# Kernel tuning notes

Measured on AMD Instinct MI355X. Metric: run time of the kernel, lower is better.

Reference implementation:

```python
import jax, jax.numpy as jnp
from jax import lax
import numpy as np

D_MODEL = 1024
D_STATE = 16    # N
D_CONV = 4     # K
EXPAND = 2
D_INNER = EXPAND * D_MODEL          # E = 2048
DT_RANK = -(-D_MODEL // 16)         # ceil(D/16) = 64
BATCH, SEQLEN = 2, 1024


def setup_inputs() -> dict:
    key = jax.random.key(0)
    ks = jax.random.split(key, 12)
    s_in = 1.0 / np.sqrt(D_MODEL)
    s_e = 1.0 / np.sqrt(D_INNER)
    s_r = 1.0 / np.sqrt(DT_RANK)
    x = jax.random.normal(ks[0], (BATCH, SEQLEN, D_MODEL), jnp.float32)
    ln_g = jnp.ones((D_MODEL,), jnp.float32)
    ln_b = jnp.zeros((D_MODEL,), jnp.float32)
    W_in = jax.random.normal(ks[1], (D_MODEL, 2 * D_INNER), jnp.float32) * s_in
    conv_w = jax.random.normal(ks[2], (D_INNER, D_CONV), jnp.float32) * (1.0 / np.sqrt(D_CONV))
    conv_b = jnp.zeros((D_INNER,), jnp.float32)
    W_xp = jax.random.normal(ks[3], (D_INNER, DT_RANK + 2 * D_STATE), jnp.float32) * s_e
    W_dt = jax.random.normal(ks[4], (DT_RANK, D_INNER), jnp.float32) * s_r
    # dt bias init so softplus(b_dt) ~ U[1e-3, 1e-1] (official mamba init)
    dt = jnp.exp(jax.random.uniform(ks[5], (D_INNER,)) * (np.log(0.1) - np.log(1e-3)) + np.log(1e-3))
    b_dt = dt + jnp.log(-jnp.expm1(-dt))  # inverse softplus
    A_log = jnp.log(jnp.broadcast_to(jnp.arange(1, D_STATE + 1, dtype=jnp.float32), (D_INNER, D_STATE)))
    D_param = jnp.ones((D_INNER,), jnp.float32)
    W_out = jax.random.normal(ks[6], (D_INNER, D_MODEL), jnp.float32) * s_e
    res_scale = jnp.ones((1,), jnp.float32)
    return dict(x=x, ln_g=ln_g, ln_b=ln_b, W_in=W_in, conv_w=conv_w, conv_b=conv_b,
                W_xp=W_xp, W_dt=W_dt, b_dt=b_dt, A_log=A_log, D_param=D_param,
                W_out=W_out, res_scale=res_scale)


def _mamba_block(x, ln_g, ln_b, W_in, conv_w, conv_b, W_xp, W_dt, b_dt,
                 A_log, D_param, W_out, res_scale):
    B, L, D = x.shape
    E, N, K, R = D_INNER, D_STATE, D_CONV, DT_RANK
    # --- prenorm (LayerNorm, eps=1e-5) ---
    mu = jnp.mean(x, axis=-1, keepdims=True)
    var = jnp.mean(jnp.square(x - mu), axis=-1, keepdims=True)
    xn = (x - mu) * lax.rsqrt(var + 1e-5) * ln_g + ln_b
    # --- in projection, split into ssm-input u and gate z ---
    xz = jnp.einsum('bld,de->ble', xn, W_in)
    u, z = jnp.split(xz, 2, axis=-1)                      # each [B,L,E]
    # --- causal depthwise conv1d over time + SiLU ---
    uc = u.transpose(0, 2, 1)                             # [B,E,L]
    conv = lax.conv_general_dilated(
        uc, conv_w[:, None, :],                           # [E,1,K]
        window_strides=(1,), padding=[(K - 1, 0)],
        feature_group_count=E,
        dimension_numbers=('NCH', 'OIH', 'NCH'))
    u2 = jax.nn.silu(conv + conv_b[None, :, None]).transpose(0, 2, 1)  # [B,L,E]
    # --- input-dependent dt, B, C ---
    x_dbl = jnp.einsum('ble,er->blr', u2, W_xp)           # [B,L,R+2N]
    dt_lo, Bm, Cm = x_dbl[..., :R], x_dbl[..., R:R + N], x_dbl[..., R + N:]
    dt = jax.nn.softplus(jnp.einsum('blr,re->ble', dt_lo, W_dt) + b_dt)  # [B,L,E]
    A = -jnp.exp(A_log)                                   # [E,N]
    # --- selective scan over time ---
    def step(h, inp):
        dt_t, B_t, C_t, u_t = inp                         # [B,E],[B,N],[B,N],[B,E]
        dA = jnp.exp(dt_t[..., None] * A)                 # [B,E,N]
        h = dA * h + (dt_t * u_t)[..., None] * B_t[:, None, :]
        y_t = jnp.einsum('ben,bn->be', h, C_t)
        return h, y_t
    h0 = jnp.zeros((B, E, N), x.dtype)
    xs = (dt.transpose(1, 0, 2), Bm.transpose(1, 0, 2),
          Cm.transpose(1, 0, 2), u2.transpose(1, 0, 2))
    _, ys = lax.scan(step, h0, xs)                        # ys: [L,B,E]
    y = ys.transpose(1, 0, 2) + u2 * D_param              # skip term D*u
    y = y * jax.nn.silu(z)                                # gating
    out = jnp.einsum('ble,ed->bld', y, W_out)
    # dropout is identity in eval mode
    return x + res_scale * out


def reference(x, ln_g, ln_b, W_in, conv_w, conv_b, W_xp, W_dt, b_dt,
              A_log, D_param, W_out, res_scale):
    return _mamba_block(x, ln_g, ln_b, W_in, conv_w, conv_b, W_xp, W_dt, b_dt,
                        A_log, D_param, W_out, res_scale)
```

## Files before the change

### kernel.cpp

```cpp
#include <hip/hip_runtime.h>
#include <hip/hip_bf16.h>

#define D_MODEL 1024
#define D_STATE 16
#define D_CONV  4
#define D_INNER 2048
#define DT_RANK 64
#define BATCH   2
#define SEQLEN  1024
#define NROWS   (BATCH * SEQLEN)
#define XDBL_W  (DT_RANK + 2 * D_STATE)
#define NCHUNK  64
#define LCHUNK  16
#define NCHAN   (BATCH * D_INNER)
#define KSPLIT_XDBL 8

typedef unsigned short ushort_t;
typedef __attribute__((ext_vector_type(8))) short bf16x8;
typedef __attribute__((ext_vector_type(8))) unsigned short ushort8v;
typedef __attribute__((ext_vector_type(4))) float f32x4;

__device__ __forceinline__ ushort_t f2bf(float f) {
    union { float f; unsigned u; } v; v.f = f;
    unsigned r = v.u + 0x7fffu + ((v.u >> 16) & 1u);
    return (ushort_t)(r >> 16);
}
__device__ __forceinline__ float bf2f(ushort_t h) {
    union { unsigned u; float f; } v; v.u = (unsigned)h << 16; return v.f;
}
__device__ __forceinline__ float fast_sigmoid(float z) {
    return __builtin_amdgcn_rcpf(1.f + __expf(-z));
}

#define PRO_LN1   2048
#define PRO_TIN1  6144
#define PRO_TOUT1 8192
#define PRO_TXP1  8448
#define PRO_TOTAL 8576

__device__ __forceinline__ void transpose_job(const float* __restrict__ W,
                                              ushort_t* __restrict__ Wt,
                                              int R, int Creal,
                                              int cx, int ry, int tid,
                                              float t[32][33])
{
    int c0 = cx * 32, r0 = ry * 32;
    int tx = tid & 31, ty = tid >> 5;
    int col = c0 + tx;
    #pragma unroll
    for (int i = 0; i < 32; i += 8) {
        float v = (col < Creal) ? W[(size_t)(r0 + ty + i) * Creal + col] : 0.f;
        t[ty + i][tx] = v;
    }
    __syncthreads();
    #pragma unroll
    for (int i = 0; i < 32; i += 8)
        Wt[(size_t)(c0 + ty + i) * R + r0 + tx] = f2bf(t[tx][ty + i]);
}

__global__ __launch_bounds__(256)
void prologue_kernel(const float* __restrict__ x, const float* __restrict__ g,
                     const float* __restrict__ bb, ushort_t* __restrict__ xnbf,
                     const float* __restrict__ W_in, ushort_t* __restrict__ WtIn,
                     const float* __restrict__ W_out, ushort_t* __restrict__ WtOut,
                     const float* __restrict__ W_xp, ushort_t* __restrict__ WtXp,
                     const float* __restrict__ W_dt, ushort_t* __restrict__ WtDt)
{
    __shared__ float t[32][33];
    __shared__ float red[8];
    int bid = blockIdx.x;
    int tid = threadIdx.x;

    if (bid < PRO_LN1) {
        const float* xr = x + (size_t)bid * D_MODEL;
        float4 v = reinterpret_cast<const float4*>(xr)[tid];
        float s  = v.x + v.y + v.z + v.w;
        float ss = v.x * v.x + v.y * v.y + v.z * v.z + v.w * v.w;
        #pragma unroll
        for (int off = 32; off; off >>= 1) {
            s  += __shfl_down(s, off);
            ss += __shfl_down(ss, off);
        }
        int wid = tid >> 6, lane = tid & 63;
        if (lane == 0) { red[wid] = s; red[4 + wid] = ss; }
        __syncthreads();
        if (tid == 0) {
            float st = 0.f, sst = 0.f;
            #pragma unroll
            for (int i = 0; i < 4; ++i) { st += red[i]; sst += red[4 + i]; }
            red[0] = st; red[4] = sst;
        }
        __syncthreads();
        float mu  = red[0] * (1.f / D_MODEL);
        float var = red[4] * (1.f / D_MODEL) - mu * mu;
        float inv = rsqrtf(var + 1e-5f);
        float4 gv = reinterpret_cast<const float4*>(g)[tid];
        float4 bv = reinterpret_cast<const float4*>(bb)[tid];
        ushort4 o;
        o.x = f2bf((v.x - mu) * inv * gv.x + bv.x);
        o.y = f2bf((v.y - mu) * inv * gv.y + bv.y);
        o.z = f2bf((v.z - mu) * inv * gv.z + bv.z);
        o.w = f2bf((v.w - mu) * inv * gv.w + bv.w);
        reinterpret_cast<ushort4*>(xnbf + (size_t)bid * D_MODEL)[tid] = o;
    } else if (bid < PRO_TIN1) {
        int j = bid - PRO_LN1;
        transpose_job(W_in, WtIn, D_MODEL, 2 * D_INNER, j & 127, j >> 7, tid, t);
    } else if (bid < PRO_TOUT1) {
        int j = bid - PRO_TIN1;
        transpose_job(W_out, WtOut, D_INNER, D_MODEL, j & 31, j >> 5, tid, t);
    } else if (bid < PRO_TXP1) {
        int j = bid - PRO_TOUT1;
        transpose_job(W_xp, WtXp, D_INNER, XDBL_W, j & 3, j >> 2, tid, t);
    } else {
        int j = bid - PRO_TXP1;
        transpose_job(W_dt, WtDt, DT_RANK, D_INNER, j & 63, j >> 6, tid, t);
    }
}

__device__ __forceinline__ void stage128x32(const ushort_t* __restrict__ gbase,
                                            size_t ld, ushort_t* ldsb, int tid)
{
    int l = tid & 63;
    int w = tid >> 6;
    int row = w * 16 + (l >> 2);
    int kg  = l & 3;
    char* lb = (char*)ldsb + w * 1024;
    const ushort_t* g0 = gbase + (size_t)row * ld + kg * 8;
    __builtin_amdgcn_global_load_lds(
        (const __attribute__((address_space(1))) unsigned*)g0,
        (__attribute__((address_space(3))) unsigned*)lb, 16, 0, 0);
    const ushort_t* g1 = g0 + (size_t)64 * ld;
    __builtin_amdgcn_global_load_lds(
        (const __attribute__((address_space(1))) unsigned*)g1,
        (__attribute__((address_space(3))) unsigned*)(lb + 4096), 16, 0, 0);
}

__device__ __forceinline__ void stage64x32(const ushort_t* __restrict__ gbase,
                                           size_t ld, ushort_t* ldsb, int tid)
{
    int l = tid & 63;
    int w = tid >> 6;
    int row = w * 16 + (l >> 2);
    int kg  = l & 3;
    char* lb = (char*)ldsb + w * 1024;
    const ushort_t* g0 = gbase + (size_t)row * ld + kg * 8;
    __builtin_amdgcn_global_load_lds(
        (const __attribute__((address_space(1))) unsigned*)g0,
        (__attribute__((address_space(3))) unsigned*)lb, 16, 0, 0);
}

__device__ __forceinline__ void stage64x64(const ushort_t* __restrict__ gbase,
                                           size_t ld, ushort_t* ldsb, int tid)
{
    int l = tid & 63;
    int w = tid >> 6;
    #pragma unroll
    for (int i = 0; i < 2; ++i) {
        int row = i * 32 + w * 8 + (l >> 3);
        const ushort_t* src = gbase + (size_t)row * ld + (l & 7) * 8;
        char* dst = (char*)ldsb + (i * 32 + w * 8) * 128;
        __builtin_amdgcn_global_load_lds(
            (const __attribute__((address_space(1))) unsigned*)src,
            (__attribute__((address_space(3))) unsigned*)dst, 16, 0, 0);
    }
}

__device__ __forceinline__ void stage128x64(const ushort_t* __restrict__ gbase,
                                            size_t ld, ushort_t* ldsb, int tid)
{
    int l = tid & 63;
    int w = tid >> 6;
    #pragma unroll
    for (int i = 0; i < 4; ++i) {
        int row = i * 32 + w * 8 + (l >> 3);
        const ushort_t* src = gbase + (size_t)row * ld + (l & 7) * 8;
        char* dst = (char*)ldsb + (i * 32 + w * 8) * 128;
        __builtin_amdgcn_global_load_lds(
            (const __attribute__((address_space(1))) unsigned*)src,
            (__attribute__((address_space(3))) unsigned*)dst, 16, 0, 0);
    }
}

__global__ __launch_bounds__(256)
void gemm_xz(const ushort_t* __restrict__ A, const ushort_t* __restrict__ Bt,
             ushort_t* __restrict__ C)
{
    __shared__ ushort_t As[128 * 64];
    __shared__ ushort_t Bs[128 * 64];
    const int K = D_MODEL, N = 2 * D_INNER;
    int bid = blockIdx.x;
    int swz = ((bid & 7) << 6) + (bid >> 3);
    int bx = swz & 31, by = swz >> 5;
    int tid = threadIdx.x;
    int l = tid & 63, wid = tid >> 6;
    int wr = wid >> 1, wc = wid & 1;
    int row0 = by * 128, col0 = bx * 128;

    f32x4 acc[4][4];
    #pragma unroll
    for (int m = 0; m < 4; ++m)
        #pragma unroll
        for (int n = 0; n < 4; ++n)
            acc[m][n] = (f32x4){0.f, 0.f, 0.f, 0.f};

    const ushort_t* Ab = A  + (size_t)row0 * K;
    const ushort_t* Bb = Bt + (size_t)col0 * K;
    int arow = wr * 64 + (l & 15);
    int brow = wc * 64 + (l & 15);
    int kb   = (l >> 4) * 8;

    for (int k0 = 0; k0 < K; k0 += 64) {
        stage128x64(Ab + k0, K, As, tid);
        stage128x64(Bb + k0, K, Bs, tid);
        __syncthreads();
        #pragma unroll
        for (int ks = 0; ks < 2; ++ks) {
            bf16x8 af[4], bfr[4];
            #pragma unroll
            for (int m = 0; m < 4; ++m)
                af[m] = *reinterpret_cast<const bf16x8*>(
                    &As[(arow + m * 16) * 64 + ks * 32 + kb]);
            #pragma unroll
            for (int n = 0; n < 4; ++n)
                bfr[n] = *reinterpret_cast<const bf16x8*>(
                    &Bs[(brow + n * 16) * 64 + ks * 32 + kb]);
            #pragma unroll
            for (int m = 0; m < 4; ++m)
                #pragma unroll
                for (int n = 0; n < 4; ++n)
                    acc[m][n] = __builtin_amdgcn_mfma_f32_16x16x32_bf16(
                        af[m], bfr[n], acc[m][n], 0, 0, 0);
        }
        __syncthreads();
    }

    int ro = (l >> 4) * 4, co = l & 15;
    #pragma unroll
    for (int m = 0; m < 4; ++m) {
        #pragma unroll
        for (int n = 0; n < 4; ++n) {
            int c = col0 + wc * 64 + n * 16 + co;
            #pragma unroll
            for (int reg = 0; reg < 4; ++reg) {
                int r = row0 + wr * 64 + m * 16 + ro + reg;
                C[(size_t)r * N + c] = f2bf(acc[m][n][reg]);
            }
        }
    }
}

__global__ __launch_bounds__(256)
void gemm_dt_fused(const float* __restrict__ parts, const ushort_t* __restrict__ Bt,
                   ushort_t* __restrict__ dtb, const float* __restrict__ bias,
                   ushort_t* __restrict__ xdblBC)
{
    __shared__ ushort_t As[128 * 32];
    __shared__ ushort_t Bs[128 * 32];
    const int K = DT_RANK;
    int tid = threadIdx.x;
    int l = tid & 63, wid = tid >> 6;
    int wr = wid >> 1, wc = wid & 1;
    int row0 = blockIdx.y * 128, col0 = blockIdx.x * 128;

    if (blockIdx.x == 0) {
        #pragma unroll
        for (int i = 0; i < 16; ++i) {
            int e2 = tid + 256 * i;
            int rr = e2 >> 5, cc = e2 & 31;
            size_t r = (size_t)(row0 + rr);
            float s = 0.f;
            #pragma unroll
            for (int z = 0; z < KSPLIT_XDBL; ++z)
                s += parts[(size_t)z * NROWS * XDBL_W + r * XDBL_W + 64 + cc];
            xdblBC[r * 32 + cc] = f2bf(s);
        }
    }

    f32x4 acc[4][4];
    #pragma unroll
    for (int m = 0; m < 4; ++m)
        #pragma unroll
        for (int n = 0; n < 4; ++n)
            acc[m][n] = (f32x4){0.f, 0.f, 0.f, 0.f};

    const ushort_t* Bb = Bt + (size_t)col0 * K;
    int arow = wr * 64 + (l & 15);
    int brow = wc * 64 + (l & 15);
    int kb   = (l >> 4) * 8;

    #pragma unroll
    for (int k0 = 0; k0 < K; k0 += 32) {
        #pragma unroll
        for (int i = 0; i < 16; ++i) {
            int e2 = tid + 256 * i;
            int rr = e2 >> 5, cc = e2 & 31;
            size_t r = (size_t)(row0 + rr);
            float s = 0.f;
            #pragma unroll
            for (int z = 0; z < KSPLIT_XDBL; ++z)
                s += parts[(size_t)z * NROWS * XDBL_W + r * XDBL_W + k0 + cc];
            As[rr * 32 + cc] = f2bf(s);
        }
        stage128x32(Bb + k0, K, Bs, tid);
        __syncthreads();
        bf16x8 af[4], bfr[4];
        #pragma unroll
        for (int m = 0; m < 4; ++m)
            af[m] = *reinterpret_cast<const bf16x8*>(&As[(arow + m * 16) * 32 + kb]);
        #pragma unroll
        for (int n = 0; n < 4; ++n)
            bfr[n] = *reinterpret_cast<const bf16x8*>(&Bs[(brow + n * 16) * 32 + kb]);
        #pragma unroll
        for (int m = 0; m < 4; ++m)
            #pragma unroll
            for (int n = 0; n < 4; ++n)
                acc[m][n] = __builtin_amdgcn_mfma_f32_16x16x32_bf16(
                    af[m], bfr[n], acc[m][n], 0, 0, 0);
        __syncthreads();
    }

    int ro = (l >> 4) * 4, co = l & 15;
    #pragma unroll
    for (int m = 0; m < 4; ++m) {
        #pragma unroll
        for (int n = 0; n < 4; ++n) {
            int c = col0 + wc * 64 + n * 16 + co;
            float bdt = bias[c];
            #pragma unroll
            for (int reg = 0; reg < 4; ++reg) {
                int r = row0 + wr * 64 + m * 16 + ro + reg;
                float v = acc[m][n][reg] + bdt;
                v = (v > 20.f) ? v : __logf(1.f + __expf(v));
                dtb[(size_t)r * D_INNER + c] = f2bf(v);
            }
        }
    }
}

__global__ __launch_bounds__(256)
void gemm_xdbl64(const ushort_t* __restrict__ A, const ushort_t* __restrict__ Bt,
                 float* __restrict__ parts)
{
    __shared__ ushort_t As[64 * 32];
    __shared__ ushort_t Bs[128 * 32];
    const int K = D_INNER;
    const int KS = D_INNER / KSPLIT_XDBL;
    int tid = threadIdx.x;
    int l = tid & 63, wid = tid >> 6;
    int wr = wid >> 1, wc = wid & 1;
    int row0 = blockIdx.y * 64;
    int kbeg = blockIdx.z * KS;

    f32x4 acc[2][4];
    #pragma unroll
    for (int m = 0; m < 2; ++m)
        #pragma unroll
        for (int n = 0; n < 4; ++n)
            acc[m][n] = (f32x4){0.f, 0.f, 0.f, 0.f};

    const ushort_t* Ab = A  + (size_t)row0 * K + kbeg;
    const ushort_t* Bb = Bt + kbeg;
    int arow = wr * 32 + (l & 15);
    int brow = wc * 64 + (l & 15);
    int kb   = (l >> 4) * 8;

    #pragma unroll
    for (int k0 = 0; k0 < KS; k0 += 32) {
        stage64x32(Ab + k0, K, As, tid);
        stage128x32(Bb + k0, K, Bs, tid);
        __syncthreads();
        bf16x8 af[2], bfr[4];
        #pragma unroll
        for (int m = 0; m < 2; ++m)
            af[m] = *reinterpret_cast<const bf16x8*>(&As[(arow + m * 16) * 32 + kb]);
        #pragma unroll
        for (int n = 0; n < 4; ++n)
            bfr[n] = *reinterpret_cast<const bf16x8*>(&Bs[(brow + n * 16) * 32 + kb]);
        #pragma unroll
        for (int m = 0; m < 2; ++m)
            #pragma unroll
            for (int n = 0; n < 4; ++n)
                acc[m][n] = __builtin_amdgcn_mfma_f32_16x16x32_bf16(
                    af[m], bfr[n], acc[m][n], 0, 0, 0);
        __syncthreads();
    }

    float* Cp = parts + (size_t)blockIdx.z * NROWS * XDBL_W;
    int ro = (l >> 4) * 4, co = l & 15;
    #pragma unroll
    for (int m = 0; m < 2; ++m) {
        #pragma unroll
        for (int n = 0; n < 4; ++n) {
            int c = wc * 64 + n * 16 + co;
            if (c >= XDBL_W) continue;
            #pragma unroll
            for (int reg = 0; reg < 4; ++reg) {
                int r = row0 + wr * 32 + m * 16 + ro + reg;
                Cp[(size_t)r * XDBL_W + c] = acc[m][n][reg];
            }
        }
    }
}

__global__ __launch_bounds__(256)
void gemm_out64(const ushort_t* __restrict__ A, const ushort_t* __restrict__ Bt,
                const float* __restrict__ x, const float* __restrict__ res_scale,
                float* __restrict__ out)
{
    __shared__ ushort_t As[64 * 64];
    __shared__ ushort_t Bs[64 * 64];
    const int K = D_INNER, N = D_MODEL;
    int bid = blockIdx.x;
    int swz = ((bid & 7) << 6) + (bid >> 3);
    int bx = swz & 15, by = swz >> 4;
    int tid = threadIdx.x;
    int l = tid & 63, wid = tid >> 6;
    int wr = wid >> 1, wc = wid & 1;
    int row0 = by * 64, col0 = bx * 64;

    f32x4 acc[2][2];
    #pragma unroll
    for (int m = 0; m < 2; ++m)
        #pragma unroll
        for (int n = 0; n < 2; ++n)
            acc[m][n] = (f32x4){0.f, 0.f, 0.f, 0.f};

    const ushort_t* Ab = A  + (size_t)row0 * K;
    const ushort_t* Bb = Bt + (size_t)col0 * K;
    int arow = wr * 32 + (l & 15);
    int brow = wc * 32 + (l & 15);
    int kb   = (l >> 4) * 8;

    for (int k0 = 0; k0 < K; k0 += 64) {
        stage64x64(Ab + k0, K, As, tid);
        stage64x64(Bb + k0, K, Bs, tid);
        __syncthreads();
        #pragma unroll
        for (int ks = 0; ks < 2; ++ks) {
            bf16x8 af[2], bfr[2];
            #pragma unroll
            for (int m = 0; m < 2; ++m)
                af[m] = *reinterpret_cast<const bf16x8*>(
                    &As[(arow + m * 16) * 64 + ks * 32 + kb]);
            #pragma unroll
            for (int n = 0; n < 2; ++n)
                bfr[n] = *reinterpret_cast<const bf16x8*>(
                    &Bs[(brow + n * 16) * 64 + ks * 32 + kb]);
            #pragma unroll
            for (int m = 0; m < 2; ++m)
                #pragma unroll
                for (int n = 0; n < 2; ++n)
                    acc[m][n] = __builtin_amdgcn_mfma_f32_16x16x32_bf16(
                        af[m], bfr[n], acc[m][n], 0, 0, 0);
        }
        __syncthreads();
    }

    float rs = res_scale[0];
    int ro = (l >> 4) * 4, co = l & 15;
    #pragma unroll
    for (int m = 0; m < 2; ++m) {
        #pragma unroll
        for (int n = 0; n < 2; ++n) {
            int c = col0 + wc * 32 + n * 16 + co;
            #pragma unroll
            for (int reg = 0; reg < 4; ++reg) {
                int r = row0 + wr * 32 + m * 16 + ro + reg;
                out[(size_t)r * N + c] = x[(size_t)r * N + c] + rs * acc[m][n][reg];
            }
        }
    }
}

__global__ __launch_bounds__(256)
void conv_silu_kernel(const ushort_t* __restrict__ xzbf, const float* __restrict__ cw,
                      const float* __restrict__ cb, ushort_t* __restrict__ u2bf)
{
    int idx4 = blockIdx.x * 256 + threadIdx.x;
    int e0 = (idx4 & 511) * 4;
    int l  = (idx4 >> 9) & (SEQLEN - 1);
    int b  = idx4 >> 19;
    size_t row = (size_t)b * SEQLEN + l;
    const ushort_t* base = xzbf + row * (2 * D_INNER) + e0;
    ushort4 r0 = {0,0,0,0}, r1 = {0,0,0,0}, r2 = {0,0,0,0}, r3;
    if (l >= 3) r0 = *reinterpret_cast<const ushort4*>(base - 3 * (size_t)(2 * D_INNER));
    if (l >= 2) r1 = *reinterpret_cast<const ushort4*>(base - 2 * (size_t)(2 * D_INNER));
    if (l >= 1) r2 = *reinterpret_cast<const ushort4*>(base - 1 * (size_t)(2 * D_INNER));
    r3 = *reinterpret_cast<const ushort4*>(base);
    const float4* cwv = reinterpret_cast<const float4*>(cw + (size_t)e0 * 4);
    float4 cb4 = *reinterpret_cast<const float4*>(cb + e0);
    const ushort_t* p0 = (const ushort_t*)&r0;
    const ushort_t* p1 = (const ushort_t*)&r1;
    const ushort_t* p2 = (const ushort_t*)&r2;
    const ushort_t* p3 = (const ushort_t*)&r3;
    const float* cbp = (const float*)&cb4;
    ushort4 o;
    ushort_t* op = (ushort_t*)&o;
    #pragma unroll
    for (int j = 0; j < 4; ++j) {
        float4 w = cwv[j];
        float a = cbp[j] + bf2f(p0[j]) * w.x + bf2f(p1[j]) * w.y
                         + bf2f(p2[j]) * w.z + bf2f(p3[j]) * w.w;
        op[j] = f2bf(a * fast_sigmoid(a));
    }
    reinterpret_cast<ushort4*>(u2bf)[idx4] = o;
}

__global__ __launch_bounds__(256)
void scan_partial_kernel(const ushort_t* __restrict__ dtb,
                         const ushort_t* __restrict__ xdblBC,
                         const ushort_t* __restrict__ u2bf,
                         const float* __restrict__ A_log,
                         ushort_t* __restrict__ hend, float* __restrict__ sumdt_buf)
{
    int idx = blockIdx.x * 256 + threadIdx.x;
    int p = idx & (NCHAN - 1);
    int c = idx >> 12;
    int b = p >> 11, e = p & (D_INNER - 1);

    float An[D_STATE];
    {
        const float4* ar = reinterpret_cast<const float4*>(A_log + (size_t)e * D_STATE);
        #pragma unroll
        for (int q = 0; q < 4; ++q) {
            float4 a4 = ar[q];
            An[q * 4 + 0] = -__expf(a4.x);
            An[q * 4 + 1] = -__expf(a4.y);
            An[q * 4 + 2] = -__expf(a4.z);
            An[q * 4 + 3] = -__expf(a4.w);
        }
    }
    float h[D_STATE];
    #pragma unroll
    for (int n = 0; n < D_STATE; ++n) h[n] = 0.f;
    float sdt = 0.f;

    size_t rowbase = (size_t)b * SEQLEN + c * LCHUNK;
    #pragma unroll
    for (int j = 0; j < LCHUNK; ++j) {
        size_t row = rowbase + j;
        float dt = bf2f(dtb[row * D_INNER + e]);
        float u  = bf2f(u2bf[row * D_INNER + e]);
        float dtu = dt * u;
        sdt += dt;
        const ushort8v* xr = reinterpret_cast<const ushort8v*>(xdblBC + row * 32);
        ushort8v b0 = xr[0], b1 = xr[1];
        float Bv[D_STATE];
        #pragma unroll
        for (int q = 0; q < 8; ++q) { Bv[q] = bf2f(b0[q]); Bv[8 + q] = bf2f(b1[q]); }
        #pragma unroll
        for (int n = 0; n < D_STATE; ++n)
            h[n] = __expf(dt * An[n]) * h[n] + dtu * Bv[n];
    }

    ushort8v o0, o1;
    #pragma unroll
    for (int q = 0; q < 8; ++q) { o0[q] = f2bf(h[q]); o1[q] = f2bf(h[8 + q]); }
    ushort8v* hp = reinterpret_cast<ushort8v*>(hend + ((size_t)p * NCHUNK + c) * D_STATE);
    hp[0] = o0; hp[1] = o1;
    sumdt_buf[p * NCHUNK + c] = sdt;
}

__global__ __launch_bounds__(1024)
void scan_combine_kernel(const float* __restrict__ A_log,
                         const float* __restrict__ sumdt_buf,
                         ushort_t* __restrict__ hend )
{
    __shared__ float Ps[NCHUNK][D_STATE];
    __shared__ float Hs[NCHUNK][D_STATE];
    int tid = threadIdx.x;
    int c = tid >> 4, n = tid & 15;
    int p = blockIdx.x;
    int e = p & (D_INNER - 1);
    float An = -__expf(A_log[e * D_STATE + n]);
    float P = __expf(An * sumdt_buf[p * NCHUNK + c]);
    float H = bf2f(hend[(size_t)p * (NCHUNK * D_STATE) + c * D_STATE + n]);
    Ps[c][n] = P; Hs[c][n] = H;
    __syncthreads();
    #pragma unroll
    for (int d = 1; d < NCHUNK; d <<= 1) {
        float Pl = 1.f, Hl = 0.f;
        if (c >= d) { Pl = Ps[c - d][n]; Hl = Hs[c - d][n]; }
        __syncthreads();
        H = P * Hl + H;
        P = P * Pl;
        Ps[c][n] = P; Hs[c][n] = H;
        __syncthreads();
    }
    float carry = (c == 0) ? 0.f : Hs[c - 1][n];
    hend[(size_t)p * (NCHUNK * D_STATE) + c * D_STATE + n] = f2bf(carry);
}

__global__ __launch_bounds__(256)
void scan_final_kernel(const ushort_t* __restrict__ dtb,
                       const ushort_t* __restrict__ xdblBC,
                       const ushort_t* __restrict__ xzbf, const ushort_t* __restrict__ u2bf,
                       ushort_t* __restrict__ ybf,
                       const float* __restrict__ A_log,
                       const float* __restrict__ D_param,
                       const ushort_t* __restrict__ hcarry)
{
    int idx = blockIdx.x * 256 + threadIdx.x;
    int p = idx & (NCHAN - 1);
    int c = idx >> 12;
    int b = p >> 11, e = p & (D_INNER - 1);
    float De = D_param[e];

    float An[D_STATE];
    {
        const float4* ar = reinterpret_cast<const float4*>(A_log + (size_t)e * D_STATE);
        #pragma unroll
        for (int q = 0; q < 4; ++q) {
            float4 a4 = ar[q];
            An[q * 4 + 0] = -__expf(a4.x);
            An[q * 4 + 1] = -__expf(a4.y);
            An[q * 4 + 2] = -__expf(a4.z);
            An[q * 4 + 3] = -__expf(a4.w);
        }
    }
    float h[D_STATE];
    {
        const ushort8v* hp = reinterpret_cast<const ushort8v*>(
            hcarry + ((size_t)p * NCHUNK + c) * D_STATE);
        ushort8v h0 = hp[0], h1 = hp[1];
        #pragma unroll
        for (int q = 0; q < 8; ++q) { h[q] = bf2f(h0[q]); h[8 + q] = bf2f(h1[q]); }
    }

    size_t rowbase = (size_t)b * SEQLEN + c * LCHUNK;
    #pragma unroll
    for (int j = 0; j < LCHUNK; ++j) {
        size_t row = rowbase + j;
        float dt = bf2f(dtb[row * D_INNER + e]);
        float u  = bf2f(u2bf[row * D_INNER + e]);
        float dtu = dt * u;
        const ushort8v* xr = reinterpret_cast<const ushort8v*>(xdblBC + row * 32);
        ushort8v b0 = xr[0], b1 = xr[1], c0v = xr[2], c1v = xr[3];
        float Bv[D_STATE], Cv[D_STATE];
        #pragma unroll
        for (int q = 0; q < 8; ++q) {
            Bv[q] = bf2f(b0[q]); Bv[8 + q] = bf2f(b1[q]);
            Cv[q] = bf2f(c0v[q]); Cv[8 + q] = bf2f(c1v[q]);
        }
        float y = 0.f;
        #pragma unroll
        for (int n = 0; n < D_STATE; ++n) {
            h[n] = __expf(dt * An[n]) * h[n] + dtu * Bv[n];
            y += h[n] * Cv[n];
        }
        float z  = bf2f(xzbf[row * (2 * D_INNER) + D_INNER + e]);
        float sz = z * fast_sigmoid(z);
        ybf[row * D_INNER + e] = f2bf((y + u * De) * sz);
    }
}

extern "C" void kernel_launch(void* const* d_in, const int* in_sizes, int n_in,
                              void* d_out, int out_size, void* d_ws, size_t ws_size,
                              hipStream_t stream)
{
    const float* x       = (const float*)d_in[0];
    const float* ln_g    = (const float*)d_in[1];
    const float* ln_b    = (const float*)d_in[2];
    const float* W_in    = (const float*)d_in[3];
    const float* conv_w  = (const float*)d_in[4];
    const float* conv_b  = (const float*)d_in[5];
    const float* W_xp    = (const float*)d_in[6];
    const float* W_dt    = (const float*)d_in[7];
    const float* b_dt    = (const float*)d_in[8];
    const float* A_log   = (const float*)d_in[9];
    const float* D_param = (const float*)d_in[10];
    const float* W_out   = (const float*)d_in[11];
    const float* res_sc  = (const float*)d_in[12];
    float* out = (float*)d_out;

    char* ws = (char*)d_ws;
    const size_t MB = 1024 * 1024;
    ushort_t* xzbf   = (ushort_t*)(ws);
    ushort_t* u2bf   = (ushort_t*)(ws + 16 * MB);
    ushort_t* dtb16  = (ushort_t*)(ws + 24 * MB);
    ushort_t* xdblBC = (ushort_t*)(ws + 32 * MB);
    ushort_t* hend   = (ushort_t*)(ws + 34 * MB);
    float*    sumdt  = (float*)(ws + 50 * MB);
    ushort_t* xnbf   = (ushort_t*)(ws + 51 * MB);
    ushort_t* WtIn   = (ushort_t*)(ws + 55 * MB);
    ushort_t* WtOut  = (ushort_t*)(ws + 63 * MB);
    ushort_t* WtXp   = (ushort_t*)(ws + 67 * MB);
    ushort_t* WtDt   = (ushort_t*)(ws + 67 * MB + 512 * 1024);
    ushort_t* ybf    = (ushort_t*)(ws + 68 * MB);
    float*    partsX = (float*)(ws + 76 * MB);

    prologue_kernel<<<PRO_TOTAL, 256, 0, stream>>>(
        x, ln_g, ln_b, xnbf, W_in, WtIn, W_out, WtOut, W_xp, WtXp, W_dt, WtDt);

    gemm_xz<<<512, 256, 0, stream>>>(xnbf, WtIn, xzbf);

    conv_silu_kernel<<<(BATCH * SEQLEN * D_INNER) / 1024, 256, 0, stream>>>(
        xzbf, conv_w, conv_b, u2bf);

    {
        dim3 grid(1, NROWS / 64, KSPLIT_XDBL);
        gemm_xdbl64<<<grid, 256, 0, stream>>>(u2bf, WtXp, partsX);
    }

    {
        dim3 grid(D_INNER / 128, NROWS / 128);
        gemm_dt_fused<<<grid, 256, 0, stream>>>(partsX, WtDt, dtb16, b_dt, xdblBC);
    }

    scan_partial_kernel<<<(NCHAN * NCHUNK) / 256, 256, 0, stream>>>(
        dtb16, xdblBC, u2bf, A_log, hend, sumdt);
    scan_combine_kernel<<<NCHAN, 1024, 0, stream>>>(A_log, sumdt, hend);
    scan_final_kernel<<<(NCHAN * NCHUNK) / 256, 256, 0, stream>>>(
        dtb16, xdblBC, xzbf, u2bf, ybf, A_log, D_param, hend);

    gemm_out64<<<512, 256, 0, stream>>>(ybf, WtOut, x, res_sc, out);
}
```

Before: 164.6 us.

## Fuse causal conv and SiLU into the in-projection GEMM epilogue

The separate conv_silu kernel is removed. The u-half tiles of the in-projection GEMM now also compute a 16-row halo with extra MFMAs, stage results in LDS, and apply the depthwise causal conv plus SiLU before writing u2 directly. This drops one kernel launch and the full write and re-read of the u half of xz. In exchange, u tiles do about 12% more MFMA work and use more LDS, and the u half of xzbf is no longer written.

```diff
diff --git a/kernel.cpp b/kernel.cpp
--- a/kernel.cpp
+++ b/kernel.cpp
@@ -181,20 +181,41 @@
     }
 }
 
+__device__ __forceinline__ void stage16x64(const ushort_t* __restrict__ gbase,
+                                           size_t ld, ushort_t* ldsb, int tid)
+{
+    int l = tid & 63;
+    int w = tid >> 6;
+    if (w < 2) {
+        int row = w * 8 + (l >> 3);
+        const ushort_t* src = gbase + (size_t)row * ld + (l & 7) * 8;
+        char* dst = (char*)ldsb + w * 8 * 128;
+        __builtin_amdgcn_global_load_lds(
+            (const __attribute__((address_space(1))) unsigned*)src,
+            (__attribute__((address_space(3))) unsigned*)dst, 16, 0, 0);
+    }
+}
+
 __global__ __launch_bounds__(256)
-void gemm_xz(const ushort_t* __restrict__ A, const ushort_t* __restrict__ Bt,
-             ushort_t* __restrict__ C)
-{
-    __shared__ ushort_t As[128 * 64];
-    __shared__ ushort_t Bs[128 * 64];
+void gemm_xz_conv(const ushort_t* __restrict__ A, const ushort_t* __restrict__ Bt,
+                  ushort_t* __restrict__ xzbf,
+                  const float* __restrict__ cw, const float* __restrict__ cb,
+                  ushort_t* __restrict__ u2bf)
+{
+    __shared__ ushort_t smem[18720];
+    ushort_t* As  = smem;
+    ushort_t* Bs  = smem + 8192;
+    ushort_t* As2 = smem + 16384;
     const int K = D_MODEL, N = 2 * D_INNER;
     int bid = blockIdx.x;
     int swz = ((bid & 7) << 6) + (bid >> 3);
     int bx = swz & 31, by = swz >> 5;
+    bool isU = (bx < 16);
     int tid = threadIdx.x;
     int l = tid & 63, wid = tid >> 6;
     int wr = wid >> 1, wc = wid & 1;
     int row0 = by * 128, col0 = bx * 128;
+    int l0 = row0 & (SEQLEN - 1);
 
     f32x4 acc[4][4];
     #pragma unroll
@@ -202,9 +223,16 @@
         #pragma unroll
         for (int n = 0; n < 4; ++n)
             acc[m][n] = (f32x4){0.f, 0.f, 0.f, 0.f};
-
-    const ushort_t* Ab = A  + (size_t)row0 * K;
-    const ushort_t* Bb = Bt + (size_t)col0 * K;
+    f32x4 acc2[4];
+    #pragma unroll
+    for (int n = 0; n < 4; ++n) acc2[n] = (f32x4){0.f, 0.f, 0.f, 0.f};
+
+    if (isU && l0 == 0)
+        reinterpret_cast<ushort4*>(As2)[tid] = (ushort4){0, 0, 0, 0};
+
+    const ushort_t* Ab  = A  + (size_t)row0 * K;
+    const ushort_t* Ab2 = A  + (size_t)(row0 - 16) * K;
+    const ushort_t* Bb  = Bt + (size_t)col0 * K;
     int arow = wr * 64 + (l & 15);
     int brow = wc * 64 + (l & 15);
     int kb   = (l >> 4) * 8;
@@ -212,6 +240,7 @@
     for (int k0 = 0; k0 < K; k0 += 64) {
         stage128x64(Ab + k0, K, As, tid);
         stage128x64(Bb + k0, K, Bs, tid);
+        if (isU && l0 != 0) stage16x64(Ab2 + k0, K, As2, tid);
         __syncthreads();
         #pragma unroll
         for (int ks = 0; ks < 2; ++ks) {
@@ -230,20 +259,67 @@
                 for (int n = 0; n < 4; ++n)
                     acc[m][n] = __builtin_amdgcn_mfma_f32_16x16x32_bf16(
                         af[m], bfr[n], acc[m][n], 0, 0, 0);
+            if (isU && wr == 0) {
+                bf16x8 af2 = *reinterpret_cast<const bf16x8*>(
+                    &As2[(l & 15) * 64 + ks * 32 + kb]);
+                #pragma unroll
+                for (int n = 0; n < 4; ++n)
+                    acc2[n] = __builtin_amdgcn_mfma_f32_16x16x32_bf16(
+                        af2, bfr[n], acc2[n], 0, 0, 0);
+            }
         }
         __syncthreads();
     }
 
     int ro = (l >> 4) * 4, co = l & 15;
-    #pragma unroll
-    for (int m = 0; m < 4; ++m) {
-        #pragma unroll
-        for (int n = 0; n < 4; ++n) {
-            int c = col0 + wc * 64 + n * 16 + co;
-            #pragma unroll
-            for (int reg = 0; reg < 4; ++reg) {
-                int r = row0 + wr * 64 + m * 16 + ro + reg;
-                C[(size_t)r * N + c] = f2bf(acc[m][n][reg]);
+    if (isU) {
+        #pragma unroll
+        for (int m = 0; m < 4; ++m)
+            #pragma unroll
+            for (int n = 0; n < 4; ++n) {
+                int c = wc * 64 + n * 16 + co;
+                #pragma unroll
+                for (int reg = 0; reg < 4; ++reg) {
+                    int r = 16 + wr * 64 + m * 16 + ro + reg;
+                    smem[r * 130 + c] = f2bf(acc[m][n][reg]);
+                }
+            }
+        if (wr == 0) {
+            #pragma unroll
+            for (int n = 0; n < 4; ++n) {
+                int c = wc * 64 + n * 16 + co;
+                #pragma unroll
+                for (int reg = 0; reg < 4; ++reg)
+                    smem[(ro + reg) * 130 + c] = f2bf(acc2[n][reg]);
+            }
+        }
+        __syncthreads();
+        int c = tid & 127;
+        int rbase = tid >> 7;
+        int e = col0 + c;
+        float4 w4 = *reinterpret_cast<const float4*>(cw + (size_t)e * 4);
+        float cbv = cb[e];
+        #pragma unroll
+        for (int i = 0; i < 64; ++i) {
+            int r = rbase + 2 * i;
+            float a = cbv
+                + bf2f(smem[(r + 13) * 130 + c]) * w4.x
+                + bf2f(smem[(r + 14) * 130 + c]) * w4.y
+                + bf2f(smem[(r + 15) * 130 + c]) * w4.z
+                + bf2f(smem[(r + 16) * 130 + c]) * w4.w;
+            u2bf[(size_t)(row0 + r) * D_INNER + e] = f2bf(a * fast_sigmoid(a));
+        }
+    } else {
+        #pragma unroll
+        for (int m = 0; m < 4; ++m) {
+            #pragma unroll
+            for (int n = 0; n < 4; ++n) {
+                int c = col0 + wc * 64 + n * 16 + co;
+                #pragma unroll
+                for (int reg = 0; reg < 4; ++reg) {
+                    int r = row0 + wr * 64 + m * 16 + ro + reg;
+                    xzbf[(size_t)r * N + c] = f2bf(acc[m][n][reg]);
+                }
             }
         }
     }
@@ -470,40 +546,6 @@
             }
         }
     }
-}
-
-__global__ __launch_bounds__(256)
-void conv_silu_kernel(const ushort_t* __restrict__ xzbf, const float* __restrict__ cw,
-                      const float* __restrict__ cb, ushort_t* __restrict__ u2bf)
-{
-    int idx4 = blockIdx.x * 256 + threadIdx.x;
-    int e0 = (idx4 & 511) * 4;
-    int l  = (idx4 >> 9) & (SEQLEN - 1);
-    int b  = idx4 >> 19;
-    size_t row = (size_t)b * SEQLEN + l;
-    const ushort_t* base = xzbf + row * (2 * D_INNER) + e0;
-    ushort4 r0 = {0,0,0,0}, r1 = {0,0,0,0}, r2 = {0,0,0,0}, r3;
-    if (l >= 3) r0 = *reinterpret_cast<const ushort4*>(base - 3 * (size_t)(2 * D_INNER));
-    if (l >= 2) r1 = *reinterpret_cast<const ushort4*>(base - 2 * (size_t)(2 * D_INNER));
-    if (l >= 1) r2 = *reinterpret_cast<const ushort4*>(base - 1 * (size_t)(2 * D_INNER));
-    r3 = *reinterpret_cast<const ushort4*>(base);
-    const float4* cwv = reinterpret_cast<const float4*>(cw + (size_t)e0 * 4);
-    float4 cb4 = *reinterpret_cast<const float4*>(cb + e0);
-    const ushort_t* p0 = (const ushort_t*)&r0;
-    const ushort_t* p1 = (const ushort_t*)&r1;
-    const ushort_t* p2 = (const ushort_t*)&r2;
-    const ushort_t* p3 = (const ushort_t*)&r3;
-    const float* cbp = (const float*)&cb4;
-    ushort4 o;
-    ushort_t* op = (ushort_t*)&o;
-    #pragma unroll
-    for (int j = 0; j < 4; ++j) {
-        float4 w = cwv[j];
-        float a = cbp[j] + bf2f(p0[j]) * w.x + bf2f(p1[j]) * w.y
-                         + bf2f(p2[j]) * w.z + bf2f(p3[j]) * w.w;
-        op[j] = f2bf(a * fast_sigmoid(a));
-    }
-    reinterpret_cast<ushort4*>(u2bf)[idx4] = o;
 }
 
 __global__ __launch_bounds__(256)
@@ -692,10 +734,8 @@
     prologue_kernel<<<PRO_TOTAL, 256, 0, stream>>>(
         x, ln_g, ln_b, xnbf, W_in, WtIn, W_out, WtOut, W_xp, WtXp, W_dt, WtDt);
 
-    gemm_xz<<<512, 256, 0, stream>>>(xnbf, WtIn, xzbf);
-
-    conv_silu_kernel<<<(BATCH * SEQLEN * D_INNER) / 1024, 256, 0, stream>>>(
-        xzbf, conv_w, conv_b, u2bf);
+    gemm_xz_conv<<<512, 256, 0, stream>>>(
+        xnbf, WtIn, xzbf, conv_w, conv_b, u2bf);
 
     {
         dim3 grid(1, NROWS / 64, KSPLIT_XDBL);
```

New measurement: 161.6 us. No clear change (-1.8%).
